# Kernel tuning notes

Hardware: AMD Instinct MI355X
Metric: run time of the kernel (lower is better)

The kernel has to match this reference:

```python
import jax, jax.numpy as jnp
import numpy as np

B, T, D = 2, 2048, 1024
H = 4
KD = int(D * 0.5)      # total key dim = 512
VD = int(D * 1.0)      # total value dim = 1024
DK, DV = KD // H, VD // H  # per-head: 128, 256
CHUNK = 64
LOW_RANK = 16          # gate_low_rank_dim
NORMALIZER = 16.0      # gate_logit_normalizer
EPS = 1e-6


def setup_inputs() -> dict:
    key = jax.random.key(0)
    ks = jax.random.split(key, 10)
    def w(k, shape):
        return jax.random.normal(k, shape, jnp.float32) / np.sqrt(shape[0]).astype(np.float32)
    return {
        "x": jax.random.normal(ks[0], (B, T, D), jnp.float32),
        "Wq": w(ks[1], (D, KD)),
        "Wk": w(ks[2], (D, KD)),
        "Wv": w(ks[3], (D, VD)),
        "Wg": w(ks[4], (D, VD)),          # output gate projection
        "Wgk1": w(ks[5], (D, LOW_RANK)),  # low-rank gate proj (no bias)
        "Wgk2": w(ks[6], (LOW_RANK, KD)),
        "bgk2": jax.random.normal(ks[7], (KD,), jnp.float32) * 0.1,
        "gnorm_w": jnp.ones((DV,), jnp.float32),  # FusedRMSNormSwishGate weight
        "Wo": w(ks[8], (VD, D)),
    }


def reference(x, Wq, Wk, Wv, Wg, Wgk1, Wgk2, bgk2, gnorm_w, Wo):
    scale = DK ** -0.5
    NC = T // CHUNK
    # [B,T,d] -> [NC,B,H,C,d_head]
    to_heads = lambda a, d: a.reshape(B, NC, CHUNK, H, d).transpose(1, 0, 3, 2, 4)
    q = to_heads(x @ Wq, DK)
    k = to_heads(x @ Wk, DK)
    v = to_heads(x @ Wv, DV)
    # per-key log decay gate: logsigmoid(low-rank proj) / normalizer
    gk = jax.nn.log_sigmoid((x @ Wgk1) @ Wgk2 + bgk2) / NORMALIZER
    G = jnp.cumsum(to_heads(gk, DK), axis=3)  # inclusive cumsum within chunk

    def chunk_step(S, inp):
        k_c, v_c, G_c = inp                       # [B,H,C,DK],[B,H,C,DV],[B,H,C,DK]
        G_last = G_c[:, :, -1, :]                 # [B,H,DK] total chunk decay
        k_bar = k_c * jnp.exp(G_last[:, :, None, :] - G_c)  # decay pos->chunk end
        S_new = jnp.exp(G_last)[..., None] * S + jnp.einsum('bhck,bhcv->bhkv', k_bar, v_c)
        return S_new, S                           # emit state at chunk START

    S0 = jnp.zeros((B, H, DK, DV), x.dtype)
    _, S_prev = jax.lax.scan(chunk_step, S0, (k, v, G))  # [NC,B,H,DK,DV]

    qg = q * jnp.exp(G) * scale                   # decay-scaled queries
    o_inter = jnp.einsum('nbhck,nbhkv->nbhcv', qg, S_prev)
    kg = k * jnp.exp(-G)
    A = jnp.einsum('nbhik,nbhjk->nbhij', qg, kg)  # intra-chunk scores
    A = jnp.where(jnp.tril(jnp.ones((CHUNK, CHUNK), bool)), A, 0.0)
    o = o_inter + jnp.einsum('nbhij,nbhjv->nbhiv', A, v)  # [NC,B,H,C,DV]
    o = o.transpose(1, 0, 3, 2, 4).reshape(B, T, H, DV)

    # fused gated RMSNorm: rmsnorm(o)*weight * swish(g), then output proj
    g = (x @ Wg).reshape(B, T, H, DV)
    o = o * jax.lax.rsqrt(jnp.mean(o * o, axis=-1, keepdims=True) + EPS) * gnorm_w
    o = o * (g * jax.nn.sigmoid(g))
    return o.reshape(B, T, VD) @ Wo
```

## Files before the change

kernel.cpp:

```cpp
#include <hip/hip_runtime.h>
#include <hip/hip_bf16.h>

#define BDIM 2
#define TDIM 2048
#define DDIM 1024
#define HH 4
#define KD 512
#define VD 1024
#define DK 128
#define DV 256
#define NC 32
#define CHUNKC 64
#define MTOT (BDIM*TDIM)
#define NALL 3584
#define STRIDE_ST ((size_t)BDIM*HH*DK*DV)

typedef __bf16 bf16x8 __attribute__((ext_vector_type(8)));
typedef float  f32x4  __attribute__((ext_vector_type(4)));
typedef __hip_bfloat16 hbf;

__device__ __forceinline__ void async_copy16(const void* g, void* l) {
  __builtin_amdgcn_global_load_lds(
      (const __attribute__((address_space(1))) void*)g,
      (__attribute__((address_space(3))) void*)l, 16, 0, 0);
}

__global__ void cast_bf16_kernel(const float* __restrict__ src, hbf* __restrict__ dst) {
  int t = blockIdx.x*256 + threadIdx.x;
  float4 v = ((const float4*)src)[t];
  union { hbf h[4]; uint2 u; } o;
  o.h[0] = __float2bfloat16(v.x); o.h[1] = __float2bfloat16(v.y);
  o.h[2] = __float2bfloat16(v.z); o.h[3] = __float2bfloat16(v.w);
  ((uint2*)dst)[t] = o.u;
}

__global__ void prep_weights(const float* __restrict__ Wq, const float* __restrict__ Wk,
                             const float* __restrict__ Wv, const float* __restrict__ Wg,
                             const float* __restrict__ Wo, const float* __restrict__ W1,
                             const float* __restrict__ W2,
                             hbf* __restrict__ wtall, hbf* __restrict__ wto) {
  __shared__ float tile[32][33];
  const int n0 = blockIdx.x*32, k0 = blockIdx.y*32;
  const int tx = threadIdx.x & 31, ty = threadIdx.x >> 5;
  if (n0 >= 1024 && n0 < 1536) {
    #pragma unroll
    for (int r = ty; r < 32; r += 8) {
      int n = n0 - 1024 + r, k = k0 + tx;
      float s = 0.f;
      #pragma unroll
      for (int j = 0; j < 16; ++j) s += W1[(size_t)k*16 + j] * W2[(size_t)j*KD + n];
      wtall[(size_t)(n0 + r)*DDIM + k] = __float2bfloat16(s);
    }
    return;
  }
  const float* W; int Nsrc, nloc; hbf* outp; int orow;
  if      (n0 < 512)  { W = Wq; Nsrc = 512;  nloc = n0;        outp = wtall; orow = n0; }
  else if (n0 < 1024) { W = Wk; Nsrc = 512;  nloc = n0 - 512;  outp = wtall; orow = n0; }
  else if (n0 < 2560) { W = Wv; Nsrc = 1024; nloc = n0 - 1536; outp = wtall; orow = n0; }
  else if (n0 < 3584) { W = Wg; Nsrc = 1024; nloc = n0 - 2560; outp = wtall; orow = n0; }
  else                { W = Wo; Nsrc = 1024; nloc = n0 - 3584; outp = wto;   orow = n0 - 3584; }
  #pragma unroll
  for (int r = ty; r < 32; r += 8)
    tile[r][tx] = W[(size_t)(k0 + r)*Nsrc + nloc + tx];
  __syncthreads();
  #pragma unroll
  for (int r = ty; r < 32; r += 8)
    outp[(size_t)(orow + r)*DDIM + k0 + tx] = __float2bfloat16(tile[tx][r]);
}

template <int MODE>
__global__ __launch_bounds__(256) void gemm_bt(const hbf* __restrict__ A,
                                               const hbf* __restrict__ Bt,
                                               float* __restrict__ Cf,
                                               hbf* __restrict__ Cq,
                                               hbf* __restrict__ Cv,
                                               int M, int N, int K) {
  __shared__ hbf As0[128][32], As1[128][32];
  __shared__ hbf Bs0[128][32], Bs1[128][32];
  const int t = threadIdx.x;
  const int w = t >> 6, l = t & 63;
  const int lr = l >> 2, lc = (l & 3)*8;
  const int lane16 = l & 15, quad = l >> 4;
  const int row0 = blockIdx.y*128, col0 = blockIdx.x*128;
  const int mb = (w >> 1)*64, nb = (w & 1)*64;

  const hbf* ga = A  + (size_t)(row0 + w*32 + lr)*K + lc;
  const hbf* gb = Bt + (size_t)(col0 + w*32 + lr)*K + lc;
  hbf* la0 = &As0[w*32][0];   hbf* la1 = &As0[w*32 + 16][0];
  hbf* la2 = &As1[w*32][0];   hbf* la3 = &As1[w*32 + 16][0];
  hbf* lb0 = &Bs0[w*32][0];   hbf* lb1 = &Bs0[w*32 + 16][0];
  hbf* lb2 = &Bs1[w*32][0];   hbf* lb3 = &Bs1[w*32 + 16][0];
  const size_t rstep = (size_t)16*K;

  f32x4 acc[4][4] = {};
  for (int k0 = 0; k0 < K; k0 += 64) {
    async_copy16(ga,              la0);
    async_copy16(ga + rstep,      la1);
    async_copy16(ga + 32,         la2);
    async_copy16(ga + rstep + 32, la3);
    async_copy16(gb,              lb0);
    async_copy16(gb + rstep,      lb1);
    async_copy16(gb + 32,         lb2);
    async_copy16(gb + rstep + 32, lb3);
    ga += 64; gb += 64;
    __syncthreads();
    {
      bf16x8 af[4], bfr[4];
      #pragma unroll
      for (int i = 0; i < 4; ++i)
        af[i] = *(const bf16x8*)&As0[mb + i*16 + lane16][quad*8];
      #pragma unroll
      for (int j = 0; j < 4; ++j)
        bfr[j] = *(const bf16x8*)&Bs0[nb + j*16 + lane16][quad*8];
      #pragma unroll
      for (int i = 0; i < 4; ++i)
        #pragma unroll
        for (int j = 0; j < 4; ++j)
          acc[i][j] = __builtin_amdgcn_mfma_f32_16x16x32_bf16(af[i], bfr[j], acc[i][j], 0, 0, 0);
    }
    {
      bf16x8 af[4], bfr[4];
      #pragma unroll
      for (int i = 0; i < 4; ++i)
        af[i] = *(const bf16x8*)&As1[mb + i*16 + lane16][quad*8];
      #pragma unroll
      for (int j = 0; j < 4; ++j)
        bfr[j] = *(const bf16x8*)&Bs1[nb + j*16 + lane16][quad*8];
      #pragma unroll
      for (int i = 0; i < 4; ++i)
        #pragma unroll
        for (int j = 0; j < 4; ++j)
          acc[i][j] = __builtin_amdgcn_mfma_f32_16x16x32_bf16(af[i], bfr[j], acc[i][j], 0, 0, 0);
    }
    __syncthreads();
  }
  #pragma unroll
  for (int i = 0; i < 4; ++i)
    #pragma unroll
    for (int j = 0; j < 4; ++j)
      #pragma unroll
      for (int r = 0; r < 4; ++r) {
        int m = row0 + mb + i*16 + quad*4 + r;
        int n = col0 + nb + j*16 + lane16;
        float v = acc[i][j][r];
        if (MODE == 0) {
          Cf[(size_t)m*N + n] = v;
        } else {
          if (col0 < 1024)       Cq[(size_t)m*1024 + n] = __float2bfloat16(v);
          else if (col0 < 1536)  Cf[(size_t)m*512  + n - 1024] = v;
          else                   Cv[(size_t)m*2048 + n - 1536] = __float2bfloat16(v);
        }
      }
}

__global__ __launch_bounds__(256) void gkcumsum_kernel(float* __restrict__ Gb,
                                                       const float* __restrict__ bias) {
  __shared__ float buf[CHUNKC][128];
  const int cs = blockIdx.x & 3;
  const int nc = (blockIdx.x >> 2) & 31;
  const int b  = blockIdx.x >> 7;
  const int t = threadIdx.x;
  const int bc = b*TDIM + nc*CHUNKC;
  const int col0 = cs*128;
  #pragma unroll
  for (int i = 0; i < 32; ++i) {
    int idx = t + 256*i;
    int c = idx >> 7, col = idx & 127;
    float s = Gb[(size_t)(bc + c)*KD + col0 + col] + bias[col0 + col];
    float ls = fminf(s, 0.f) - log1pf(expf(-fabsf(s)));
    buf[c][col] = ls * (1.0f/16.0f);
  }
  __syncthreads();
  if (t < 128) {
    float acc = 0.f;
    #pragma unroll
    for (int c = 0; c < CHUNKC; ++c) {
      acc += buf[c][t];
      buf[c][t] = acc;
    }
  }
  __syncthreads();
  #pragma unroll
  for (int i = 0; i < 32; ++i) {
    int idx = t + 256*i;
    int c = idx >> 7, col = idx & 127;
    Gb[(size_t)(bc + c)*KD + col0 + col] = buf[c][col];
  }
}

__global__ __launch_bounds__(256) void state_chunk_kernel(const hbf* __restrict__ qkbf,
                                                          const hbf* __restrict__ vgbf,
                                                          const float* __restrict__ Gb,
                                                          hbf* __restrict__ Ub,
                                                          float* __restrict__ dec) {
  const int bh = blockIdx.x & 7;
  const int nc = blockIdx.x >> 3;
  const int b = bh >> 2, h = bh & 3;
  const int t = threadIdx.x;
  const int w = t >> 6, l = t & 63;
  const int lane16 = l & 15, quad = l >> 4;
  __shared__ hbf kbarT[DK][72];
  __shared__ hbf vT[DV][72];
  __shared__ float glast[DK];
  const int bc = b*TDIM + nc*CHUNKC;
  if (t < DK) {
    float gl = Gb[(size_t)(bc + 63)*KD + h*DK + t];
    glast[t] = gl;
    dec[((size_t)nc*8 + bh)*DK + t] = expf(gl);
  }
  __syncthreads();
  #pragma unroll
  for (int i = 0; i < 32; ++i) {
    int idx = t + 256*i;
    int c = idx >> 7, kk = idx & 127;
    float g  = Gb[(size_t)(bc + c)*KD + h*DK + kk];
    float kv = __bfloat162float(qkbf[(size_t)(bc + c)*1024 + 512 + h*DK + kk]);
    kbarT[kk][c] = __float2bfloat16(kv * expf(glast[kk] - g));
  }
  #pragma unroll
  for (int i = 0; i < 64; ++i) {
    int idx = t + 256*i;
    int c = idx >> 8, col = idx & 255;
    vT[col][c] = vgbf[(size_t)(bc + c)*2048 + h*DV + col];
  }
  __syncthreads();
  f32x4 acc[4][8] = {};
  #pragma unroll
  for (int kc = 0; kc < 2; ++kc) {
    bf16x8 av[4], bk[8];
    #pragma unroll
    for (int i = 0; i < 4; ++i)
      av[i] = *(const bf16x8*)&vT[w*64 + i*16 + lane16][kc*32 + quad*8];
    #pragma unroll
    for (int j = 0; j < 8; ++j)
      bk[j] = *(const bf16x8*)&kbarT[j*16 + lane16][kc*32 + quad*8];
    #pragma unroll
    for (int i = 0; i < 4; ++i)
      #pragma unroll
      for (int j = 0; j < 8; ++j)
        acc[i][j] = __builtin_amdgcn_mfma_f32_16x16x32_bf16(av[i], bk[j], acc[i][j], 0, 0, 0);
  }
  hbf* ub = Ub + ((size_t)nc*8 + bh)*((size_t)DK*DV);
  #pragma unroll
  for (int i = 0; i < 4; ++i)
    #pragma unroll
    for (int j = 0; j < 8; ++j)
      #pragma unroll
      for (int r = 0; r < 4; ++r) {
        int v = w*64 + i*16 + quad*4 + r;
        int k = j*16 + lane16;
        ub[(size_t)v*DK + k] = __float2bfloat16(acc[i][j][r]);
      }
}

__global__ __launch_bounds__(256) void state_scan_kernel(const hbf* __restrict__ Ub,
                                                         const float* __restrict__ dec,
                                                         hbf* __restrict__ Spb) {
  const int p = blockIdx.x*256 + threadIdx.x;
  const size_t e = (size_t)p*2;
  const int k = (int)(e & 127);
  const int bh = (int)(e >> 15);
  float S0 = 0.f, S1 = 0.f;
  for (int nc = 0; nc < NC; ++nc) {
    const size_t off = (size_t)nc*STRIDE_ST + e;
    uint uu = *(const uint*)(Ub + off);
    hbf u0 = *(const hbf*)&uu;
    hbf u1 = *((const hbf*)&uu + 1);
    union { hbf h[2]; uint u; } ov;
    ov.h[0] = __float2bfloat16(S0); ov.h[1] = __float2bfloat16(S1);
    *(uint*)(Spb + off) = ov.u;
    float2 d = *(const float2*)(dec + ((size_t)nc*8 + bh)*DK + k);
    S0 = S0 * d.x + __bfloat162float(u0);
    S1 = S1 * d.y + __bfloat162float(u1);
  }
}

__global__ __launch_bounds__(256) void out_kernel(const hbf* __restrict__ qkbf,
                                                  const hbf* __restrict__ vgbf,
                                                  const float* __restrict__ Gb,
                                                  const hbf* __restrict__ Spb,
                                                  const float* __restrict__ gnw,
                                                  hbf* __restrict__ obf) {
  const int blk = blockIdx.x;
  const int h = blk & 3, b = (blk >> 2) & 1, nc = blk >> 3;
  const int t = threadIdx.x;
  const int w = t >> 6, l = t & 63;
  const int lane16 = l & 15, quad = l >> 4;

  __shared__ __align__(16) unsigned char smem[64768];
  hbf (*qgs)[136] = (hbf(*)[136])(smem);
  hbf (*Ald)[72]  = (hbf(*)[72]) (smem + 17408);
  hbf (*kgs)[136] = (hbf(*)[136])(smem + 26624);
  hbf (*vT)[72]   = (hbf(*)[72]) (smem + 26624);
  float* ssum     = (float*)     (smem + 63488);
  float* invb     = (float*)     (smem + 64512);

  const float scale = 0.088388347648318447f;
  const int bc = b*TDIM + nc*CHUNKC;

  #pragma unroll
  for (int i = 0; i < 32; ++i) {
    int idx = t + 256*i;
    int c = idx >> 7, kk = idx & 127;
    float g = Gb[(size_t)(bc + c)*KD + h*DK + kk];
    float qv = __bfloat162float(qkbf[(size_t)(bc + c)*1024 + h*DK + kk]);
    float kv = __bfloat162float(qkbf[(size_t)(bc + c)*1024 + 512 + h*DK + kk]);
    qgs[c][kk] = __float2bfloat16(qv * expf(g) * scale);
    kgs[c][kk] = __float2bfloat16(kv * expf(-g));
  }
  __syncthreads();

  f32x4 acc1[4] = {};
  #pragma unroll
  for (int kc = 0; kc < 4; ++kc) {
    bf16x8 af = *(const bf16x8*)&qgs[w*16 + lane16][kc*32 + quad*8];
    #pragma unroll
    for (int j = 0; j < 4; ++j) {
      bf16x8 bf = *(const bf16x8*)&kgs[j*16 + lane16][kc*32 + quad*8];
      acc1[j] = __builtin_amdgcn_mfma_f32_16x16x32_bf16(af, bf, acc1[j], 0, 0, 0);
    }
  }
  __syncthreads();

  #pragma unroll
  for (int j = 0; j < 4; ++j)
    #pragma unroll
    for (int r = 0; r < 4; ++r) {
      int cr = w*16 + quad*4 + r;
      int cc = j*16 + lane16;
      Ald[cr][cc] = __float2bfloat16(cc <= cr ? acc1[j][r] : 0.f);
    }
  #pragma unroll
  for (int i = 0; i < 64; ++i) {
    int e = t + 256*i;
    int c = e >> 8, col = e & 255;
    vT[col][c] = vgbf[(size_t)(bc + c)*2048 + h*DV + col];
  }
  __syncthreads();

  const hbf* SpB = Spb + ((size_t)nc*8 + (b*HH + h))*((size_t)DK*DV);
  f32x4 acc[4][4] = {};
  #pragma unroll
  for (int kc = 0; kc < 4; ++kc) {
    bf16x8 af[4], bs[4];
    #pragma unroll
    for (int i = 0; i < 4; ++i)
      af[i] = *(const bf16x8*)&qgs[i*16 + lane16][kc*32 + quad*8];
    #pragma unroll
    for (int j = 0; j < 4; ++j) {
      int n = w*64 + j*16 + lane16;
      bs[j] = *(const bf16x8*)(SpB + (size_t)n*DK + kc*32 + quad*8);
    }
    #pragma unroll
    for (int i = 0; i < 4; ++i)
      #pragma unroll
      for (int j = 0; j < 4; ++j)
        acc[i][j] = __builtin_amdgcn_mfma_f32_16x16x32_bf16(af[i], bs[j], acc[i][j], 0, 0, 0);
  }
  #pragma unroll
  for (int kc = 0; kc < 2; ++kc) {
    bf16x8 aa[4], bv[4];
    #pragma unroll
    for (int i = 0; i < 4; ++i)
      aa[i] = *(const bf16x8*)&Ald[i*16 + lane16][kc*32 + quad*8];
    #pragma unroll
    for (int j = 0; j < 4; ++j)
      bv[j] = *(const bf16x8*)&vT[w*64 + j*16 + lane16][kc*32 + quad*8];
    #pragma unroll
    for (int i = 0; i < 4; ++i)
      #pragma unroll
      for (int j = 0; j < 4; ++j)
        acc[i][j] = __builtin_amdgcn_mfma_f32_16x16x32_bf16(aa[i], bv[j], acc[i][j], 0, 0, 0);
  }

  #pragma unroll
  for (int i = 0; i < 4; ++i)
    #pragma unroll
    for (int r = 0; r < 4; ++r) {
      float s = 0.f;
      #pragma unroll
      for (int j = 0; j < 4; ++j) s += acc[i][j][r]*acc[i][j][r];
      s += __shfl_xor(s, 1); s += __shfl_xor(s, 2);
      s += __shfl_xor(s, 4); s += __shfl_xor(s, 8);
      if (lane16 == 0) ssum[(i*16 + quad*4 + r)*4 + w] = s;
    }
  __syncthreads();
  if (t < 64) {
    float tot = ssum[t*4] + ssum[t*4+1] + ssum[t*4+2] + ssum[t*4+3];
    invb[t] = rsqrtf(tot * (1.0f/DV) + 1e-6f);
  }
  __syncthreads();
  float gnwv[4];
  #pragma unroll
  for (int j = 0; j < 4; ++j) gnwv[j] = gnw[w*64 + j*16 + lane16];
  #pragma unroll
  for (int i = 0; i < 4; ++i)
    #pragma unroll
    for (int r = 0; r < 4; ++r) {
      int m = i*16 + quad*4 + r;
      float inv = invb[m];
      size_t grow_ = (size_t)(bc + m)*2048 + 1024 + h*DV + w*64;
      size_t orow_ = (size_t)(bc + m)*VD + h*DV + w*64;
      #pragma unroll
      for (int j = 0; j < 4; ++j) {
        float gv = __bfloat162float(vgbf[grow_ + j*16 + lane16]);
        float sig = 1.f / (1.f + expf(-gv));
        float val = acc[i][j][r] * inv * gnwv[j];
        obf[orow_ + j*16 + lane16] = __float2bfloat16(val * (gv * sig));
      }
    }
}

extern "C" void kernel_launch(void* const* d_in, const int* in_sizes, int n_in,
                              void* d_out, int out_size, void* d_ws, size_t ws_size,
                              hipStream_t stream) {
  const float* x    = (const float*)d_in[0];
  const float* Wq   = (const float*)d_in[1];
  const float* Wk   = (const float*)d_in[2];
  const float* Wv   = (const float*)d_in[3];
  const float* Wg   = (const float*)d_in[4];
  const float* Wgk1 = (const float*)d_in[5];
  const float* Wgk2 = (const float*)d_in[6];
  const float* bgk2 = (const float*)d_in[7];
  const float* gnw  = (const float*)d_in[8];
  const float* Wo   = (const float*)d_in[9];
  float* out = (float*)d_out;

  float* ws  = (float*)d_ws;
  float* Gb  = ws;
  float* dec = Gb  + (size_t)MTOT*KD;
  hbf* xbf   = (hbf*)(dec + (size_t)NC*BDIM*HH*DK);
  hbf* wtall = xbf   + (size_t)MTOT*DDIM;
  hbf* wto   = wtall + (size_t)NALL*DDIM;
  hbf* qkbf  = wto   + (size_t)DDIM*DDIM;
  hbf* vgbf  = qkbf  + (size_t)MTOT*1024;
  hbf* Ub    = vgbf  + (size_t)MTOT*2048;
  hbf* Spb   = Ub    + (size_t)NC*STRIDE_ST;
  hbf* obf   = Ub;

  cast_bf16_kernel<<<MTOT*DDIM/4/256, 256, 0, stream>>>(x, xbf);
  prep_weights<<<dim3(144, 32), 256, 0, stream>>>(Wq, Wk, Wv, Wg, Wo, Wgk1, Wgk2, wtall, wto);

  gemm_bt<1><<<dim3(NALL/128, MTOT/128), 256, 0, stream>>>(xbf, wtall, Gb, qkbf, vgbf, MTOT, NALL, DDIM);

  gkcumsum_kernel<<<256, 256, 0, stream>>>(Gb, bgk2);
  state_chunk_kernel<<<NC*BDIM*HH, 256, 0, stream>>>(qkbf, vgbf, Gb, Ub, dec);
  state_scan_kernel<<<(int)(STRIDE_ST/2/256), 256, 0, stream>>>(Ub, dec, Spb);
  out_kernel<<<NC*BDIM*HH, 256, 0, stream>>>(qkbf, vgbf, Gb, Spb, gnw, obf);
  gemm_bt<0><<<dim3(DDIM/128, MTOT/128), 256, 0, stream>>>(obf, wto, out, (hbf*)nullptr, (hbf*)nullptr, MTOT, DDIM, DDIM);
}
```

Measured before the change: 230.3 us.

## Widen projection GEMM tile to 128x256 and swizzle LDS columns in GEMMs

The fused projection GEMM moves into a dedicated kernel with 128x256 output tiles, so each wave computes 4x8 MFMA blocks and every A-tile load is reused across twice as many columns. Both GEMMs also rotate the 16-byte column chunk by row group when copying into shared memory and reading from it, to cut LDS bank conflicts on the fragment loads. The wider tile raises accumulator register use and LDS footprint, which can lower occupancy, and the projection grid shrinks to 14x32 blocks.

Result: slower. 259.1 us (+12.5%).

```diff
diff --git a/kernel.cpp b/kernel.cpp
--- a/kernel.cpp
+++ b/kernel.cpp
@@ -68,24 +68,105 @@
     outp[(size_t)(orow + r)*DDIM + k0 + tx] = __float2bfloat16(tile[tx][r]);
 }
 
-template <int MODE>
+
+__global__ __launch_bounds__(256) void gemm_proj(const hbf* __restrict__ A,
+                                                 const hbf* __restrict__ Bt,
+                                                 float* __restrict__ Cf,
+                                                 hbf* __restrict__ Cq,
+                                                 hbf* __restrict__ Cv) {
+  const int K = DDIM;
+  __shared__ hbf As0[128][32], As1[128][32];
+  __shared__ hbf Bs0[256][32], Bs1[256][32];
+  const int t = threadIdx.x;
+  const int w = t >> 6, l = t & 63;
+  const int lr = l >> 2;
+  const int srcc = (((l & 3) - (l >> 4)) & 3) * 8;
+  const int lane16 = l & 15, quad = l >> 4;
+  const int sw = ((lane16 >> 2)) & 3;
+  const int row0 = blockIdx.y*128, col0 = blockIdx.x*256;
+  const int mb = (w >> 1)*64, nb = (w & 1)*128;
+
+  const hbf* ga = A  + (size_t)(row0 + w*32 + lr)*K + srcc;
+  const hbf* gb = Bt + (size_t)(col0 + w*64 + lr)*K + srcc;
+  hbf* la0 = &As0[w*32][0];   hbf* la1 = &As0[w*32 + 16][0];
+  hbf* la2 = &As1[w*32][0];   hbf* la3 = &As1[w*32 + 16][0];
+  const size_t rstep = (size_t)16*K;
+
+  f32x4 acc[4][8] = {};
+  for (int k0 = 0; k0 < K; k0 += 64) {
+    async_copy16(ga,              la0);
+    async_copy16(ga + rstep,      la1);
+    async_copy16(ga + 32,         la2);
+    async_copy16(ga + rstep + 32, la3);
+    #pragma unroll
+    for (int rr = 0; rr < 4; ++rr) {
+      async_copy16(gb + rstep*rr,      &Bs0[w*64 + rr*16][0]);
+      async_copy16(gb + rstep*rr + 32, &Bs1[w*64 + rr*16][0]);
+    }
+    ga += 64; gb += 64;
+    __syncthreads();
+    {
+      bf16x8 af[4], bfr[8];
+      #pragma unroll
+      for (int i = 0; i < 4; ++i)
+        af[i] = *(const bf16x8*)&As0[mb + i*16 + lane16][((quad + sw) & 3)*8];
+      #pragma unroll
+      for (int j = 0; j < 8; ++j)
+        bfr[j] = *(const bf16x8*)&Bs0[nb + j*16 + lane16][((quad + sw) & 3)*8];
+      #pragma unroll
+      for (int i = 0; i < 4; ++i)
+        #pragma unroll
+        for (int j = 0; j < 8; ++j)
+          acc[i][j] = __builtin_amdgcn_mfma_f32_16x16x32_bf16(af[i], bfr[j], acc[i][j], 0, 0, 0);
+    }
+    {
+      bf16x8 af[4], bfr[8];
+      #pragma unroll
+      for (int i = 0; i < 4; ++i)
+        af[i] = *(const bf16x8*)&As1[mb + i*16 + lane16][((quad + sw) & 3)*8];
+      #pragma unroll
+      for (int j = 0; j < 8; ++j)
+        bfr[j] = *(const bf16x8*)&Bs1[nb + j*16 + lane16][((quad + sw) & 3)*8];
+      #pragma unroll
+      for (int i = 0; i < 4; ++i)
+        #pragma unroll
+        for (int j = 0; j < 8; ++j)
+          acc[i][j] = __builtin_amdgcn_mfma_f32_16x16x32_bf16(af[i], bfr[j], acc[i][j], 0, 0, 0);
+    }
+    __syncthreads();
+  }
+  #pragma unroll
+  for (int i = 0; i < 4; ++i)
+    #pragma unroll
+    for (int j = 0; j < 8; ++j)
+      #pragma unroll
+      for (int r = 0; r < 4; ++r) {
+        int m = row0 + mb + i*16 + quad*4 + r;
+        int n = col0 + nb + j*16 + lane16;
+        float v = acc[i][j][r];
+        if (n < 1024)       Cq[(size_t)m*1024 + n] = __float2bfloat16(v);
+        else if (n < 1536)  Cf[(size_t)m*512  + n - 1024] = v;
+        else                Cv[(size_t)m*2048 + n - 1536] = __float2bfloat16(v);
+      }
+}
+
 __global__ __launch_bounds__(256) void gemm_bt(const hbf* __restrict__ A,
                                                const hbf* __restrict__ Bt,
                                                float* __restrict__ Cf,
-                                               hbf* __restrict__ Cq,
-                                               hbf* __restrict__ Cv,
                                                int M, int N, int K) {
   __shared__ hbf As0[128][32], As1[128][32];
   __shared__ hbf Bs0[128][32], Bs1[128][32];
   const int t = threadIdx.x;
   const int w = t >> 6, l = t & 63;
-  const int lr = l >> 2, lc = (l & 3)*8;
+  const int lr = l >> 2;
+  const int srcc = (((l & 3) - (l >> 4)) & 3) * 8;
   const int lane16 = l & 15, quad = l >> 4;
+  const int sw = (lane16 >> 2) & 3;
   const int row0 = blockIdx.y*128, col0 = blockIdx.x*128;
   const int mb = (w >> 1)*64, nb = (w & 1)*64;
 
-  const hbf* ga = A  + (size_t)(row0 + w*32 + lr)*K + lc;
-  const hbf* gb = Bt + (size_t)(col0 + w*32 + lr)*K + lc;
+  const hbf* ga = A  + (size_t)(row0 + w*32 + lr)*K + srcc;
+  const hbf* gb = Bt + (size_t)(col0 + w*32 + lr)*K + srcc;
   hbf* la0 = &As0[w*32][0];   hbf* la1 = &As0[w*32 + 16][0];
   hbf* la2 = &As1[w*32][0];   hbf* la3 = &As1[w*32 + 16][0];
   hbf* lb0 = &Bs0[w*32][0];   hbf* lb1 = &Bs0[w*32 + 16][0];
@@ -108,10 +189,10 @@
       bf16x8 af[4], bfr[4];
       #pragma unroll
       for (int i = 0; i < 4; ++i)
-        af[i] = *(const bf16x8*)&As0[mb + i*16 + lane16][quad*8];
+        af[i] = *(const bf16x8*)&As0[mb + i*16 + lane16][((quad + sw) & 3)*8];
       #pragma unroll
       for (int j = 0; j < 4; ++j)
-        bfr[j] = *(const bf16x8*)&Bs0[nb + j*16 + lane16][quad*8];
+        bfr[j] = *(const bf16x8*)&Bs0[nb + j*16 + lane16][((quad + sw) & 3)*8];
       #pragma unroll
       for (int i = 0; i < 4; ++i)
         #pragma unroll
@@ -122,10 +203,10 @@
       bf16x8 af[4], bfr[4];
       #pragma unroll
       for (int i = 0; i < 4; ++i)
-        af[i] = *(const bf16x8*)&As1[mb + i*16 + lane16][quad*8];
+        af[i] = *(const bf16x8*)&As1[mb + i*16 + lane16][((quad + sw) & 3)*8];
       #pragma unroll
       for (int j = 0; j < 4; ++j)
-        bfr[j] = *(const bf16x8*)&Bs1[nb + j*16 + lane16][quad*8];
+        bfr[j] = *(const bf16x8*)&Bs1[nb + j*16 + lane16][((quad + sw) & 3)*8];
       #pragma unroll
       for (int i = 0; i < 4; ++i)
         #pragma unroll
@@ -142,14 +223,7 @@
       for (int r = 0; r < 4; ++r) {
         int m = row0 + mb + i*16 + quad*4 + r;
         int n = col0 + nb + j*16 + lane16;
-        float v = acc[i][j][r];
-        if (MODE == 0) {
-          Cf[(size_t)m*N + n] = v;
-        } else {
-          if (col0 < 1024)       Cq[(size_t)m*1024 + n] = __float2bfloat16(v);
-          else if (col0 < 1536)  Cf[(size_t)m*512  + n - 1024] = v;
-          else                   Cv[(size_t)m*2048 + n - 1536] = __float2bfloat16(v);
-        }
+        Cf[(size_t)m*N + n] = acc[i][j][r];
       }
 }
 
@@ -441,11 +515,11 @@
   cast_bf16_kernel<<<MTOT*DDIM/4/256, 256, 0, stream>>>(x, xbf);
   prep_weights<<<dim3(144, 32), 256, 0, stream>>>(Wq, Wk, Wv, Wg, Wo, Wgk1, Wgk2, wtall, wto);
 
-  gemm_bt<1><<<dim3(NALL/128, MTOT/128), 256, 0, stream>>>(xbf, wtall, Gb, qkbf, vgbf, MTOT, NALL, DDIM);
+  gemm_proj<<<dim3(NALL/256, MTOT/128), 256, 0, stream>>>(xbf, wtall, Gb, qkbf, vgbf);
 
   gkcumsum_kernel<<<256, 256, 0, stream>>>(Gb, bgk2);
   state_chunk_kernel<<<NC*BDIM*HH, 256, 0, stream>>>(qkbf, vgbf, Gb, Ub, dec);
   state_scan_kernel<<<(int)(STRIDE_ST/2/256), 256, 0, stream>>>(Ub, dec, Spb);
   out_kernel<<<NC*BDIM*HH, 256, 0, stream>>>(qkbf, vgbf, Gb, Spb, gnw, obf);
-  gemm_bt<0><<<dim3(DDIM/128, MTOT/128), 256, 0, stream>>>(obf, wto, out, (hbf*)nullptr, (hbf*)nullptr, MTOT, DDIM, DDIM);
-}
+  gemm_bt<<<dim3(DDIM/128, MTOT/128), 256, 0, stream>>>(obf, wto, out, MTOT, DDIM, DDIM);
+}
```

## Swizzle GEMM LDS layout and precompute decayed q/k/kbar in gate kernel

Applied to the files above, without the earlier changes.

The GEMM now rotates the 16-byte column slot per row group when staging tiles into LDS, and reads back with the matching rotation, to reduce LDS bank conflicts on the MFMA fragment loads. The gate cumsum kernel also computes exp(G)-scaled queries, exp(-G) keys, chunk-end-decayed keys, and the per-chunk decay vector. These are stored in bf16, so the state and output kernels only copy preformatted tiles instead of reloading fp32 G and recomputing exponentials. This adds three extra bf16 buffers of global traffic but removes duplicated fp32 reads and transcendental work.

Measured after the change: 231.0 us. About the same (+0.3%).

```diff
diff --git a/kernel.cpp b/kernel.cpp
--- a/kernel.cpp
+++ b/kernel.cpp
@@ -79,13 +79,15 @@
   __shared__ hbf Bs0[128][32], Bs1[128][32];
   const int t = threadIdx.x;
   const int w = t >> 6, l = t & 63;
-  const int lr = l >> 2, lc = (l & 3)*8;
+  const int lr = l >> 2;
+  const int srcc = (((l & 3) - (l >> 4)) & 3) * 8;
   const int lane16 = l & 15, quad = l >> 4;
+  const int sw = (lane16 >> 2) & 3;
   const int row0 = blockIdx.y*128, col0 = blockIdx.x*128;
   const int mb = (w >> 1)*64, nb = (w & 1)*64;
 
-  const hbf* ga = A  + (size_t)(row0 + w*32 + lr)*K + lc;
-  const hbf* gb = Bt + (size_t)(col0 + w*32 + lr)*K + lc;
+  const hbf* ga = A  + (size_t)(row0 + w*32 + lr)*K + srcc;
+  const hbf* gb = Bt + (size_t)(col0 + w*32 + lr)*K + srcc;
   hbf* la0 = &As0[w*32][0];   hbf* la1 = &As0[w*32 + 16][0];
   hbf* la2 = &As1[w*32][0];   hbf* la3 = &As1[w*32 + 16][0];
   hbf* lb0 = &Bs0[w*32][0];   hbf* lb1 = &Bs0[w*32 + 16][0];
@@ -108,10 +110,10 @@
       bf16x8 af[4], bfr[4];
       #pragma unroll
       for (int i = 0; i < 4; ++i)
-        af[i] = *(const bf16x8*)&As0[mb + i*16 + lane16][quad*8];
+        af[i] = *(const bf16x8*)&As0[mb + i*16 + lane16][((quad + sw) & 3)*8];
       #pragma unroll
       for (int j = 0; j < 4; ++j)
-        bfr[j] = *(const bf16x8*)&Bs0[nb + j*16 + lane16][quad*8];
+        bfr[j] = *(const bf16x8*)&Bs0[nb + j*16 + lane16][((quad + sw) & 3)*8];
       #pragma unroll
       for (int i = 0; i < 4; ++i)
         #pragma unroll
@@ -122,10 +124,10 @@
       bf16x8 af[4], bfr[4];
       #pragma unroll
       for (int i = 0; i < 4; ++i)
-        af[i] = *(const bf16x8*)&As1[mb + i*16 + lane16][quad*8];
+        af[i] = *(const bf16x8*)&As1[mb + i*16 + lane16][((quad + sw) & 3)*8];
       #pragma unroll
       for (int j = 0; j < 4; ++j)
-        bfr[j] = *(const bf16x8*)&Bs1[nb + j*16 + lane16][quad*8];
+        bfr[j] = *(const bf16x8*)&Bs1[nb + j*16 + lane16][((quad + sw) & 3)*8];
       #pragma unroll
       for (int i = 0; i < 4; ++i)
         #pragma unroll
@@ -146,53 +148,73 @@
         if (MODE == 0) {
           Cf[(size_t)m*N + n] = v;
         } else {
-          if (col0 < 1024)       Cq[(size_t)m*1024 + n] = __float2bfloat16(v);
-          else if (col0 < 1536)  Cf[(size_t)m*512  + n - 1024] = v;
-          else                   Cv[(size_t)m*2048 + n - 1536] = __float2bfloat16(v);
+          if (n < 1024)       Cq[(size_t)m*1024 + n] = __float2bfloat16(v);
+          else if (n < 1536)  Cf[(size_t)m*512  + n - 1024] = v;
+          else                Cv[(size_t)m*2048 + n - 1536] = __float2bfloat16(v);
         }
       }
 }
 
-__global__ __launch_bounds__(256) void gkcumsum_kernel(float* __restrict__ Gb,
-                                                       const float* __restrict__ bias) {
+__global__ __launch_bounds__(256) void gate_kernel(const float* __restrict__ Gpre,
+                                                   const hbf* __restrict__ qkbf,
+                                                   const float* __restrict__ bias,
+                                                   hbf* __restrict__ qgb,
+                                                   hbf* __restrict__ kgb,
+                                                   hbf* __restrict__ kbarb,
+                                                   float* __restrict__ dec) {
   __shared__ float buf[CHUNKC][128];
-  const int cs = blockIdx.x & 3;
+  const int h  = blockIdx.x & 3;
   const int nc = (blockIdx.x >> 2) & 31;
   const int b  = blockIdx.x >> 7;
   const int t = threadIdx.x;
   const int bc = b*TDIM + nc*CHUNKC;
-  const int col0 = cs*128;
+  const int col0 = h*128;
   #pragma unroll
   for (int i = 0; i < 32; ++i) {
     int idx = t + 256*i;
     int c = idx >> 7, col = idx & 127;
-    float s = Gb[(size_t)(bc + c)*KD + col0 + col] + bias[col0 + col];
-    float ls = fminf(s, 0.f) - log1pf(expf(-fabsf(s)));
-    buf[c][col] = ls * (1.0f/16.0f);
+    float s = Gpre[(size_t)(bc + c)*KD + col0 + col] + bias[col0 + col];
+    buf[c][col] = (fminf(s, 0.f) - log1pf(expf(-fabsf(s)))) * (1.0f/16.0f);
   }
   __syncthreads();
   if (t < 128) {
     float acc = 0.f;
     #pragma unroll
-    for (int c = 0; c < CHUNKC; ++c) {
-      acc += buf[c][t];
-      buf[c][t] = acc;
-    }
-  }
-  __syncthreads();
-  #pragma unroll
-  for (int i = 0; i < 32; ++i) {
+    for (int c = 0; c < CHUNKC; ++c) { acc += buf[c][t]; buf[c][t] = acc; }
+    dec[((size_t)nc*8 + b*HH + h)*DK + t] = expf(acc);
+  }
+  __syncthreads();
+  const float scale = 0.088388347648318447f;
+  #pragma unroll
+  for (int i = 0; i < 16; ++i) {
     int idx = t + 256*i;
-    int c = idx >> 7, col = idx & 127;
-    Gb[(size_t)(bc + c)*KD + col0 + col] = buf[c][col];
-  }
-}
-
-__global__ __launch_bounds__(256) void state_chunk_kernel(const hbf* __restrict__ qkbf,
+    int c = idx >> 6, cp = (idx & 63)*2;
+    float g0 = buf[c][cp], g1 = buf[c][cp + 1];
+    float gl0 = buf[63][cp], gl1 = buf[63][cp + 1];
+    const size_t qoff = (size_t)(bc + c)*1024 + col0 + cp;
+    uint qu = *(const uint*)(qkbf + qoff);
+    uint ku = *(const uint*)(qkbf + qoff + 512);
+    float q0 = __bfloat162float(((const hbf*)&qu)[0]);
+    float q1 = __bfloat162float(((const hbf*)&qu)[1]);
+    float k0 = __bfloat162float(((const hbf*)&ku)[0]);
+    float k1 = __bfloat162float(((const hbf*)&ku)[1]);
+    union { hbf h2[2]; uint u; } o1, o2, o3;
+    o1.h2[0] = __float2bfloat16(q0 * expf(g0) * scale);
+    o1.h2[1] = __float2bfloat16(q1 * expf(g1) * scale);
+    o2.h2[0] = __float2bfloat16(k0 * expf(-g0));
+    o2.h2[1] = __float2bfloat16(k1 * expf(-g1));
+    o3.h2[0] = __float2bfloat16(k0 * expf(gl0 - g0));
+    o3.h2[1] = __float2bfloat16(k1 * expf(gl1 - g1));
+    const size_t ooff = (size_t)(bc + c)*KD + col0 + cp;
+    *(uint*)(qgb + ooff)   = o1.u;
+    *(uint*)(kgb + ooff)   = o2.u;
+    *(uint*)(kbarb + ooff) = o3.u;
+  }
+}
+
+__global__ __launch_bounds__(256) void state_chunk_kernel(const hbf* __restrict__ kbarb,
                                                           const hbf* __restrict__ vgbf,
-                                                          const float* __restrict__ Gb,
-                                                          hbf* __restrict__ Ub,
-                                                          float* __restrict__ dec) {
+                                                          hbf* __restrict__ Ub) {
   const int bh = blockIdx.x & 7;
   const int nc = blockIdx.x >> 3;
   const int b = bh >> 2, h = bh & 3;
@@ -201,21 +223,12 @@
   const int lane16 = l & 15, quad = l >> 4;
   __shared__ hbf kbarT[DK][72];
   __shared__ hbf vT[DV][72];
-  __shared__ float glast[DK];
   const int bc = b*TDIM + nc*CHUNKC;
-  if (t < DK) {
-    float gl = Gb[(size_t)(bc + 63)*KD + h*DK + t];
-    glast[t] = gl;
-    dec[((size_t)nc*8 + bh)*DK + t] = expf(gl);
-  }
-  __syncthreads();
   #pragma unroll
   for (int i = 0; i < 32; ++i) {
     int idx = t + 256*i;
     int c = idx >> 7, kk = idx & 127;
-    float g  = Gb[(size_t)(bc + c)*KD + h*DK + kk];
-    float kv = __bfloat162float(qkbf[(size_t)(bc + c)*1024 + 512 + h*DK + kk]);
-    kbarT[kk][c] = __float2bfloat16(kv * expf(glast[kk] - g));
+    kbarT[kk][c] = kbarb[(size_t)(bc + c)*KD + h*DK + kk];
   }
   #pragma unroll
   for (int i = 0; i < 64; ++i) {
@@ -275,9 +288,9 @@
   }
 }
 
-__global__ __launch_bounds__(256) void out_kernel(const hbf* __restrict__ qkbf,
+__global__ __launch_bounds__(256) void out_kernel(const hbf* __restrict__ qgb,
+                                                  const hbf* __restrict__ kgb,
                                                   const hbf* __restrict__ vgbf,
-                                                  const float* __restrict__ Gb,
                                                   const hbf* __restrict__ Spb,
                                                   const float* __restrict__ gnw,
                                                   hbf* __restrict__ obf) {
@@ -295,18 +308,14 @@
   float* ssum     = (float*)     (smem + 63488);
   float* invb     = (float*)     (smem + 64512);
 
-  const float scale = 0.088388347648318447f;
   const int bc = b*TDIM + nc*CHUNKC;
 
   #pragma unroll
-  for (int i = 0; i < 32; ++i) {
+  for (int i = 0; i < 4; ++i) {
     int idx = t + 256*i;
-    int c = idx >> 7, kk = idx & 127;
-    float g = Gb[(size_t)(bc + c)*KD + h*DK + kk];
-    float qv = __bfloat162float(qkbf[(size_t)(bc + c)*1024 + h*DK + kk]);
-    float kv = __bfloat162float(qkbf[(size_t)(bc + c)*1024 + 512 + h*DK + kk]);
-    qgs[c][kk] = __float2bfloat16(qv * expf(g) * scale);
-    kgs[c][kk] = __float2bfloat16(kv * expf(-g));
+    int c = idx >> 4, ch = (idx & 15)*8;
+    *(uint4*)&qgs[c][ch] = *(const uint4*)(qgb + (size_t)(bc + c)*KD + h*DK + ch);
+    *(uint4*)&kgs[c][ch] = *(const uint4*)(kgb + (size_t)(bc + c)*KD + h*DK + ch);
   }
   __syncthreads();
 
@@ -434,7 +443,10 @@
   hbf* wto   = wtall + (size_t)NALL*DDIM;
   hbf* qkbf  = wto   + (size_t)DDIM*DDIM;
   hbf* vgbf  = qkbf  + (size_t)MTOT*1024;
-  hbf* Ub    = vgbf  + (size_t)MTOT*2048;
+  hbf* qgb   = vgbf  + (size_t)MTOT*2048;
+  hbf* kgb   = qgb   + (size_t)MTOT*KD;
+  hbf* kbarb = kgb   + (size_t)MTOT*KD;
+  hbf* Ub    = kbarb + (size_t)MTOT*KD;
   hbf* Spb   = Ub    + (size_t)NC*STRIDE_ST;
   hbf* obf   = Ub;
 
@@ -443,9 +455,9 @@
 
   gemm_bt<1><<<dim3(NALL/128, MTOT/128), 256, 0, stream>>>(xbf, wtall, Gb, qkbf, vgbf, MTOT, NALL, DDIM);
 
-  gkcumsum_kernel<<<256, 256, 0, stream>>>(Gb, bgk2);
-  state_chunk_kernel<<<NC*BDIM*HH, 256, 0, stream>>>(qkbf, vgbf, Gb, Ub, dec);
+  gate_kernel<<<256, 256, 0, stream>>>(Gb, qkbf, bgk2, qgb, kgb, kbarb, dec);
+  state_chunk_kernel<<<NC*BDIM*HH, 256, 0, stream>>>(kbarb, vgbf, Ub);
   state_scan_kernel<<<(int)(STRIDE_ST/2/256), 256, 0, stream>>>(Ub, dec, Spb);
-  out_kernel<<<NC*BDIM*HH, 256, 0, stream>>>(qkbf, vgbf, Gb, Spb, gnw, obf);
+  out_kernel<<<NC*BDIM*HH, 256, 0, stream>>>(qgb, kgb, vgbf, Spb, gnw, obf);
   gemm_bt<0><<<dim3(DDIM/128, MTOT/128), 256, 0, stream>>>(obf, wto, out, (hbf*)nullptr, (hbf*)nullptr, MTOT, DDIM, DDIM);
 }
```
